# Kernel tuning notes

Hardware: AMD Instinct MI355X
Metric: run time of the kernel (lower is better)

Reference implementation:

```python
import jax, jax.numpy as jnp
import numpy as np

T, B, DX, DH, DZ, K = 128, 256, 64, 512, 128, 16


def _lin(x, W, b):
    return x @ W.T + b


def _forget_mult(F, Z, h0):
    # C[t] = F[t]*Z[t] + (1-F[t])*C[t-1], C[-1] = h0; shapes (T,B,H)
    def step(c, fz):
        f, z = fz
        c = f * z + (1.0 - f) * c
        return c, c
    _, C = jax.lax.scan(step, h0, (F, Z))
    return C


def _qrnn_layer(X, W, b, h0):
    # window=1, output_gate=True, zoneout=0 (eval)
    Y = _lin(X, W, b)                      # (T,B,3H)
    Z, F, O = jnp.split(Y, 3, axis=-1)
    C = _forget_mult(jax.nn.sigmoid(F), jnp.tanh(Z), h0)
    return jax.nn.sigmoid(O) * C           # H


def _planar_flow(z, u, w, b):
    # z: (B,T,Dz); u,w: (K,Dz); b: (K,). Returns z_K and summed log-det.
    def m(x):
        return jax.nn.softplus(x) - 1.0
    def step(carry, p):
        z, sldj = carry
        uk, wk, bk = p
        udw = jnp.dot(uk, wk)
        w_hat = wk / jnp.linalg.norm(wk)
        u_hat = (m(udw) - udw) * w_hat + uk
        t = jnp.tanh(z @ wk + bk)          # (B,T)
        z = z + u_hat * t[..., None]
        psi_u = (1.0 - t * t) * jnp.dot(wk, u_hat)
        sldj = sldj - jnp.log(jnp.abs(psi_u + 1.0) + 1e-8)
        return (z, sldj), None
    sldj0 = jnp.zeros(z.shape[:-1], z.dtype)
    (zK, sldj), _ = jax.lax.scan(step, (z, sldj0), (u, w, b))
    return zK, sldj


def _forward(x, y, eps, hs_W, hs_b, q_W, q_b, enc_phi_W, enc_phi_b,
             enc_mean_W, enc_mean_b, enc_std_W, enc_std_b,
             prior_phi_W, prior_phi_b, prior_mean_W, prior_mean_b,
             prior_std_W, prior_std_b, dec_phi_W1, dec_phi_b1,
             dec_phi_W2, dec_phi_b2, dec_mean_W, dec_mean_b,
             dec_std_W, dec_std_b, pnf_u, pnf_w, pnf_b):
    Bsz = x.shape[1]
    Dh = hs_W.shape[0] // 3
    h0 = jnp.zeros((Bsz, Dh), x.dtype)
    # hidden-state QRNN over x
    h = _qrnn_layer(x, hs_W, hs_b, h0)                 # (T,B,Dh)
    # inference QRNN over reversed [y, h]
    rev_in = jnp.concatenate([jnp.flip(y, 0), jnp.flip(h, 0)], axis=-1)
    a = _qrnn_layer(rev_in, q_W, q_b, h0)              # (T,B,Dh)
    rev_a = jnp.swapaxes(jnp.flip(a, 0), 0, 1)         # (B,T,Dh)
    # encoder
    e = jax.nn.relu(_lin(rev_a, enc_phi_W[0], enc_phi_b[0]))
    e = jax.nn.relu(_lin(e, enc_phi_W[1], enc_phi_b[1]))
    enc_mean = jax.nn.sigmoid(_lin(e, enc_mean_W, enc_mean_b))   # (B,T,Dz)
    enc_std = jax.nn.softplus(_lin(e, enc_std_W, enc_std_b))
    z0 = enc_mean + enc_std * eps
    z_k, sldj = _planar_flow(z0, pnf_u, pnf_w, pnf_b)
    # prior
    hp = jnp.swapaxes(h, 0, 1)                          # (B,T,Dh)
    p = jax.nn.relu(_lin(hp, prior_phi_W[0], prior_phi_b[0]))
    p = jax.nn.relu(_lin(p, prior_phi_W[1], prior_phi_b[1]))
    prior_mean = jax.nn.sigmoid(_lin(p, prior_mean_W, prior_mean_b))
    prior_std = jax.nn.softplus(_lin(p, prior_std_W, prior_std_b))
    # decoder
    d = jax.nn.relu(_lin(jnp.concatenate([z_k, hp], axis=-1), dec_phi_W1, dec_phi_b1))
    d = jax.nn.relu(_lin(d, dec_phi_W2, dec_phi_b2))
    dec_mean = jax.nn.sigmoid(_lin(d, dec_mean_W, dec_mean_b))   # (B,T,Dx)
    dec_std = jax.nn.softplus(_lin(d, dec_std_W, dec_std_b))
    return dec_mean, dec_std, enc_mean, enc_std, prior_mean, prior_std, z_k, sldj


def setup_inputs() -> dict:
    key = jax.random.key(0)
    ks = jax.random.split(key, 20)
    def w(i, shape, scale=0.05):
        return (jax.random.normal(ks[i], shape) * scale).astype(jnp.float32)
    return {
        "x": w(0, (T, B, DX), 1.0),
        "y": w(1, (T, B, DX), 1.0),
        "eps": w(2, (B, T, DZ), 1.0),
        "hs_W": w(3, (3 * DH, DX)), "hs_b": jnp.zeros((3 * DH,), jnp.float32),
        "q_W": w(4, (3 * DH, DX + DH)), "q_b": jnp.zeros((3 * DH,), jnp.float32),
        "enc_phi_W": w(5, (2, DH, DH)), "enc_phi_b": jnp.zeros((2, DH), jnp.float32),
        "enc_mean_W": w(6, (DZ, DH)), "enc_mean_b": jnp.zeros((DZ,), jnp.float32),
        "enc_std_W": w(7, (DZ, DH)), "enc_std_b": jnp.zeros((DZ,), jnp.float32),
        "prior_phi_W": w(8, (2, DH, DH)), "prior_phi_b": jnp.zeros((2, DH), jnp.float32),
        "prior_mean_W": w(9, (DZ, DH)), "prior_mean_b": jnp.zeros((DZ,), jnp.float32),
        "prior_std_W": w(10, (DZ, DH)), "prior_std_b": jnp.zeros((DZ,), jnp.float32),
        "dec_phi_W1": w(11, (DH, DH + DZ)), "dec_phi_b1": jnp.zeros((DH,), jnp.float32),
        "dec_phi_W2": w(12, (DH, DH)), "dec_phi_b2": jnp.zeros((DH,), jnp.float32),
        "dec_mean_W": w(13, (DX, DH)), "dec_mean_b": jnp.zeros((DX,), jnp.float32),
        "dec_std_W": w(14, (DX, DH)), "dec_std_b": jnp.zeros((DX,), jnp.float32),
        "pnf_u": w(15, (K, DZ), 0.01), "pnf_w": w(16, (K, DZ), 0.01), "pnf_b": w(17, (K,), 0.01),
    }


def reference(x, y, eps, hs_W, hs_b, q_W, q_b, enc_phi_W, enc_phi_b,
              enc_mean_W, enc_mean_b, enc_std_W, enc_std_b,
              prior_phi_W, prior_phi_b, prior_mean_W, prior_mean_b,
              prior_std_W, prior_std_b, dec_phi_W1, dec_phi_b1,
              dec_phi_W2, dec_phi_b2, dec_mean_W, dec_mean_b,
              dec_std_W, dec_std_b, pnf_u, pnf_w, pnf_b):
    return _forward(x, y, eps, hs_W, hs_b, q_W, q_b, enc_phi_W, enc_phi_b,
                    enc_mean_W, enc_mean_b, enc_std_W, enc_std_b,
                    prior_phi_W, prior_phi_b, prior_mean_W, prior_mean_b,
                    prior_std_W, prior_std_b, dec_phi_W1, dec_phi_b1,
                    dec_phi_W2, dec_phi_b2, dec_mean_W, dec_mean_b,
                    dec_std_W, dec_std_b, pnf_u, pnf_w, pnf_b)
```

## Files before the change

### kernel.cpp

```cpp
#include <hip/hip_runtime.h>
#include <cstddef>
#include <cstdint>

#define DEVI __device__ __forceinline__

namespace {

typedef _Float16 f16;
typedef _Float16 half4 __attribute__((ext_vector_type(4)));
typedef _Float16 half8 __attribute__((ext_vector_type(8)));
typedef _Float16 f16x2 __attribute__((ext_vector_type(2)));
typedef float floatx16 __attribute__((ext_vector_type(16)));

typedef const __attribute__((address_space(1))) void gvoid;
typedef __attribute__((address_space(3))) void lvoid;
#define GLL(gp, lp) __builtin_amdgcn_global_load_lds((gvoid*)(gp), (lvoid*)(lp), 16, 0, 0)

constexpr float kLog2e = 1.4426950408889634f;
constexpr float kLn2   = 0.6931471805599453f;
DEVI float fexp2_(float x) { return __builtin_amdgcn_exp2f(x); }
DEVI float frcp_(float x)  { return __builtin_amdgcn_rcpf(x); }
DEVI float flog2_(float x) { return __builtin_amdgcn_logf(x); }
DEVI float fsig_(float v)  { return frcp_(1.f + fexp2_(-kLog2e * v)); }
DEVI float ftanh_(float v) { return 1.f - 2.f * frcp_(1.f + fexp2_(2.f * kLog2e * v)); }
DEVI float fsoftplus_(float v) {
  return fmaxf(v, 0.f) + kLn2 * flog2_(1.f + fexp2_(-kLog2e * fabsf(v)));
}

struct CvtTab { const float* s[14]; f16* d[14]; int n4[14]; };

__global__ __launch_bounds__(256)
void cvt_k(CvtTab tab) {
  const int e = blockIdx.y;
  const int n4 = tab.n4[e];
  const float4* s = (const float4*)tab.s[e];
  f16* d = tab.d[e];
  for (int i = blockIdx.x * 256 + threadIdx.x; i < n4; i += gridDim.x * 256) {
    const float4 v = s[i];
    half4 o = {(f16)v.x, (f16)v.y, (f16)v.z, (f16)v.w};
    *(half4*)(d + (size_t)i * 4) = o;
  }
}

template <int AM, int OM>
__global__ __launch_bounds__(256)
void gemm16_k(const f16* __restrict__ A0, const f16* __restrict__ A1,
              const f16* __restrict__ W0, const f16* __restrict__ W1,
              const float* __restrict__ bias, const float* __restrict__ bias2,
              float* __restrict__ C, float* __restrict__ C2,
              f16* __restrict__ Ch, int N, int K, int lda) {
  __shared__ __align__(16) char lds[65536];
  const int tid = threadIdx.x;
  const int l = tid & 63, w = tid >> 6;
  const int m0 = blockIdx.y * 128, n0 = blockIdx.x * 128;
  const int Nh = N >> 1;

  const f16* pa[4]; const f16* pa2[4]; const f16* pb[4];
#pragma unroll
  for (int r = 0; r < 4; ++r) {
    const int s = w * 256 + r * 64 + l;
    const int row = s >> 3, c = s & 7;
    const int kc8 = (c ^ (row & 7)) * 8;
    const int m = m0 + row;
    if constexpr (AM == 0) {
      pa[r] = A0 + (size_t)m * lda + kc8;
      pa2[r] = nullptr;
    } else if constexpr (AM == 1) {
      const int t = m >> 8, b = m & 255;
      pa[r]  = A0 + (size_t)((127 - t) * 256 + b) * 64 + kc8;
      pa2[r] = A1 + (size_t)((b << 7) | (127 - t)) * 512 + kc8;
    } else {
      pa[r]  = A0 + (size_t)m * 128 + kc8;
      pa2[r] = A1 + (size_t)m * 512 + kc8;
    }
    const int n = n0 + row;
    if constexpr (OM == 2) {
      pb[r] = (n < Nh ? W0 + (size_t)n * K : W1 + (size_t)(n - Nh) * K) + kc8;
    } else {
      pb[r] = W0 + (size_t)n * K + kc8;
    }
  }

  const int wr0 = (w >> 1) * 64, wc0 = (w & 1) * 64;
  int offA[2][4], offB[2][4];
#pragma unroll
  for (int mi = 0; mi < 2; ++mi) {
    const int row = wr0 + mi * 32 + (l & 31);
#pragma unroll
    for (int s16 = 0; s16 < 4; ++s16) {
      const int c = (s16 * 2 + (l >> 5)) ^ (row & 7);
      offA[mi][s16] = row * 128 + c * 16;
    }
  }
#pragma unroll
  for (int nj = 0; nj < 2; ++nj) {
    const int row = wc0 + nj * 32 + (l & 31);
#pragma unroll
    for (int s16 = 0; s16 < 4; ++s16) {
      const int c = (s16 * 2 + (l >> 5)) ^ (row & 7);
      offB[nj][s16] = row * 128 + c * 16;
    }
  }

  float bv[2];
#pragma unroll
  for (int nj = 0; nj < 2; ++nj) {
    const int gcol = n0 + wc0 + nj * 32 + (l & 31);
    if constexpr (OM == 2) {
      bv[nj] = (gcol >= Nh) ? bias2[gcol - Nh] : bias[gcol];
    } else {
      bv[nj] = bias[gcol];
    }
  }
  asm volatile("" : "+v"(bv[0]), "+v"(bv[1]));
  asm volatile("s_waitcnt vmcnt(0)" ::: "memory");

  auto stage = [&](int st, int buf) {
    char* dA = lds + buf * 32768;
    char* dB = dA + 16384;
#pragma unroll
    for (int r = 0; r < 4; ++r) {
      const f16* ga;
      if constexpr (AM == 0)      ga = pa[r] + st * 64;
      else if constexpr (AM == 1) ga = (st == 0) ? pa[r] : (pa2[r] + (st - 1) * 64);
      else                        ga = (st < 2) ? (pa[r] + st * 64) : (pa2[r] + (st - 2) * 64);
      GLL(ga, dA + (w * 256 + r * 64) * 16);
      GLL(pb[r] + st * 64, dB + (w * 256 + r * 64) * 16);
    }
  };

  floatx16 acc[2][2] = {};
  const int nsteps = K >> 6;
  stage(0, 0);
  for (int st = 0; st < nsteps; ++st) {
    const int cur = st & 1;
    if (st + 1 < nsteps) {
      stage(st + 1, cur ^ 1);
      asm volatile("s_waitcnt vmcnt(8)" ::: "memory");
    } else {
      asm volatile("s_waitcnt vmcnt(0)" ::: "memory");
    }
    __builtin_amdgcn_s_barrier();
    __builtin_amdgcn_sched_barrier(0);
    const char* cA = lds + cur * 32768;
    const char* cB = cA + 16384;
#pragma unroll
    for (int s16 = 0; s16 < 4; ++s16) {
      const half8 a0 = *(const half8*)(cA + offA[0][s16]);
      const half8 a1 = *(const half8*)(cA + offA[1][s16]);
      const half8 b0 = *(const half8*)(cB + offB[0][s16]);
      const half8 b1 = *(const half8*)(cB + offB[1][s16]);
      acc[0][0] = __builtin_amdgcn_mfma_f32_32x32x16_f16(a0, b0, acc[0][0], 0, 0, 0);
      acc[0][1] = __builtin_amdgcn_mfma_f32_32x32x16_f16(a0, b1, acc[0][1], 0, 0, 0);
      acc[1][0] = __builtin_amdgcn_mfma_f32_32x32x16_f16(a1, b0, acc[1][0], 0, 0, 0);
      acc[1][1] = __builtin_amdgcn_mfma_f32_32x32x16_f16(a1, b1, acc[1][1], 0, 0, 0);
    }
    __builtin_amdgcn_sched_barrier(0);
    asm volatile("s_waitcnt lgkmcnt(0)" ::: "memory");
    __builtin_amdgcn_s_barrier();
  }

  const int col_l = l & 31;
#pragma unroll
  for (int nj = 0; nj < 2; ++nj) {
    const int gcol = n0 + wc0 + nj * 32 + col_l;
    if constexpr (OM == 2) {
      const bool second = gcol >= Nh;
      float* cp = second ? C2 : C;
      const int cl = second ? gcol - Nh : gcol;
#pragma unroll
      for (int mi = 0; mi < 2; ++mi) {
#pragma unroll
        for (int reg = 0; reg < 16; ++reg) {
          const int rl = (reg & 3) + 8 * (reg >> 2) + 4 * (l >> 5);
          const int grow = m0 + wr0 + mi * 32 + rl;
          const float v = acc[mi][nj][reg] + bv[nj];
          cp[(size_t)grow * Nh + cl] = second ? fsoftplus_(v) : fsig_(v);
        }
      }
    } else {
#pragma unroll
      for (int mi = 0; mi < 2; ++mi) {
#pragma unroll
        for (int reg = 0; reg < 16; ++reg) {
          const int rl = (reg & 3) + 8 * (reg >> 2) + 4 * (l >> 5);
          const int grow = m0 + wr0 + mi * 32 + rl;
          const float v = acc[mi][nj][reg] + bv[nj];
          float rr;
          if constexpr (OM == 0) rr = (gcol < 512) ? ftanh_(v) : fsig_(v);
          else                   rr = fmaxf(v, 0.f);
          Ch[(size_t)grow * N + gcol] = (f16)rr;
        }
      }
    }
  }
}

template <int MODE>
__global__ __launch_bounds__(256)
void scan_k(const f16* __restrict__ Y, f16* __restrict__ H1) {
  const int idx = blockIdx.x * 256 + threadIdx.x;
  const int b = idx >> 8;
  const int h0 = (idx & 255) * 2;
  float c0 = 0.f, c1 = 0.f;
  for (int t = 0; t < 128; ++t) {
    const f16* p = Y + (size_t)(t * 256 + b) * 1536 + h0;
    const f16x2 zv = *(const f16x2*)(p);
    const f16x2 fv = *(const f16x2*)(p + 512);
    const f16x2 ov = *(const f16x2*)(p + 1024);
    const float f0 = (float)fv[0], f1 = (float)fv[1];
    c0 = f0 * (float)zv[0] + (1.f - f0) * c0;
    c1 = f1 * (float)zv[1] + (1.f - f1) * c1;
    f16x2 hv = {(f16)((float)ov[0] * c0), (f16)((float)ov[1] * c1)};
    const int tt = (MODE == 0) ? t : (127 - t);
    *(f16x2*)(H1 + (size_t)((b << 7) | tt) * 512 + h0) = hv;
  }
}

__global__ __launch_bounds__(256)
void z0_k(const float* __restrict__ mean, const float* __restrict__ sd,
          const float* __restrict__ eps, float* __restrict__ z) {
  const int i = blockIdx.x * 256 + threadIdx.x;
  const float4 m = ((const float4*)mean)[i];
  const float4 s = ((const float4*)sd)[i];
  const float4 e = ((const float4*)eps)[i];
  ((float4*)z)[i] = make_float4(m.x + s.x * e.x, m.y + s.y * e.y,
                                m.z + s.z * e.z, m.w + s.w * e.w);
}

__global__ __launch_bounds__(64)
void flow_pre_k(const float* __restrict__ u, const float* __restrict__ w,
                float* __restrict__ uhat, float* __restrict__ wu) {
  const int k = blockIdx.x, l = threadIdx.x;
  const float w0 = w[k * 128 + l], w1 = w[k * 128 + 64 + l];
  const float u0 = u[k * 128 + l], u1 = u[k * 128 + 64 + l];
  float nrm = w0 * w0 + w1 * w1;
  float udw = u0 * w0 + u1 * w1;
#pragma unroll
  for (int o = 32; o; o >>= 1) { nrm += __shfl_xor(nrm, o); udw += __shfl_xor(udw, o); }
  const float inv = 1.f / sqrtf(nrm);
  const float coef = (fsoftplus_(udw) - 1.f) - udw;
  const float uh0 = coef * (w0 * inv) + u0;
  const float uh1 = coef * (w1 * inv) + u1;
  uhat[k * 128 + l] = uh0;
  uhat[k * 128 + 64 + l] = uh1;
  float dwu = w0 * uh0 + w1 * uh1;
#pragma unroll
  for (int o = 32; o; o >>= 1) dwu += __shfl_xor(dwu, o);
  if (l == 0) wu[k] = dwu;
}

__global__ __launch_bounds__(256)
void flow_k(float* __restrict__ z, const float* __restrict__ w,
            const float* __restrict__ b, const float* __restrict__ uhat,
            const float* __restrict__ wu, float* __restrict__ sldj,
            f16* __restrict__ zh) {
  const int row = blockIdx.x * 4 + (threadIdx.x >> 6);
  const int l = threadIdx.x & 63;
  float* zp = z + (size_t)row * 128;
  float z0 = zp[l], z1 = zp[64 + l];
  float sl = 0.f;
#pragma unroll
  for (int k = 0; k < 16; ++k) {
    const float w0 = w[k * 128 + l], w1 = w[k * 128 + 64 + l];
    float s = z0 * w0 + z1 * w1;
#pragma unroll
    for (int o = 32; o; o >>= 1) s += __shfl_xor(s, o);
    const float t = ftanh_(s + b[k]);
    z0 += uhat[k * 128 + l] * t;
    z1 += uhat[k * 128 + 64 + l] * t;
    const float psi = (1.f - t * t) * wu[k];
    sl -= kLn2 * flog2_(fabsf(psi + 1.f) + 1e-8f);
  }
  zp[l] = z0;
  zp[64 + l] = z1;
  zh[(size_t)row * 128 + l] = (f16)z0;
  zh[(size_t)row * 128 + 64 + l] = (f16)z1;
  if (l == 0) sldj[row] = sl;
}

}

extern "C" void kernel_launch(void* const* d_in, const int* in_sizes, int n_in,
                              void* d_out, int out_size, void* d_ws, size_t ws_size,
                              hipStream_t stream) {
  const float* x           = (const float*)d_in[0];
  const float* y           = (const float*)d_in[1];
  const float* eps         = (const float*)d_in[2];
  const float* hs_b        = (const float*)d_in[4];
  const float* q_b         = (const float*)d_in[6];
  const float* enc_phi_b   = (const float*)d_in[8];
  const float* enc_mean_b  = (const float*)d_in[10];
  const float* enc_std_b   = (const float*)d_in[12];
  const float* prior_phi_b = (const float*)d_in[14];
  const float* prior_mean_b= (const float*)d_in[16];
  const float* prior_std_b = (const float*)d_in[18];
  const float* dec_b1      = (const float*)d_in[20];
  const float* dec_b2      = (const float*)d_in[22];
  const float* dec_mean_b  = (const float*)d_in[24];
  const float* dec_std_b   = (const float*)d_in[26];
  const float* pnf_u       = (const float*)d_in[27];
  const float* pnf_w       = (const float*)d_in[28];
  const float* pnf_b       = (const float*)d_in[29];

  float* out = (float*)d_out;
  float* dec_mean  = out;
  float* dec_std   = out + 2097152;
  float* enc_mean  = out + 4194304;
  float* enc_std   = out + 8388608;
  float* prior_mean= out + 12582912;
  float* prior_std = out + 16777216;
  float* zk        = out + 20971520;
  float* sldj      = out + 25165824;

  char* ws = (char*)d_ws;
  f16* Ybuf  = (f16*)(ws + 0);
  f16* e1    = (f16*)(ws + 0);
  f16* e2    = (f16*)(ws + 33554432);
  f16* arev  = (f16*)(ws + 100663296);
  f16* h_bt  = (f16*)(ws + 134217728);
  f16* zk_h  = (f16*)(ws + 167772160);
  f16* xh    = (f16*)(ws + 176160768);
  f16* yh    = (f16*)(ws + 180355072);
  f16* wbuf  = (f16*)(ws + 184549376);
  float* uhat= (float*)(ws + 190447616);
  float* wu  = (float*)(ws + 190455808);

  f16* w_hs   = wbuf + 0;
  f16* w_q    = wbuf + 98304;
  f16* w_ephi = wbuf + 983040;
  f16* w_emean= wbuf + 1507328;
  f16* w_estd = wbuf + 1572864;
  f16* w_pphi = wbuf + 1638400;
  f16* w_pmean= wbuf + 2162688;
  f16* w_pstd = wbuf + 2228224;
  f16* w_d1   = wbuf + 2293760;
  f16* w_d2   = wbuf + 2621440;
  f16* w_dmean= wbuf + 2883584;
  f16* w_dstd = wbuf + 2916352;

  CvtTab tab;
  const float* srcs[14] = {x, y, (const float*)d_in[3], (const float*)d_in[5],
                           (const float*)d_in[7], (const float*)d_in[9],
                           (const float*)d_in[11], (const float*)d_in[13],
                           (const float*)d_in[15], (const float*)d_in[17],
                           (const float*)d_in[19], (const float*)d_in[21],
                           (const float*)d_in[23], (const float*)d_in[25]};
  f16* dsts[14] = {xh, yh, w_hs, w_q, w_ephi, w_emean, w_estd, w_pphi,
                   w_pmean, w_pstd, w_d1, w_d2, w_dmean, w_dstd};
  const int ns[14] = {2097152, 2097152, 98304, 884736, 524288, 65536, 65536,
                      524288, 65536, 65536, 327680, 262144, 32768, 32768};
  for (int i = 0; i < 14; ++i) { tab.s[i] = srcs[i]; tab.d[i] = dsts[i]; tab.n4[i] = ns[i] >> 2; }
  cvt_k<<<dim3(128, 14), 256, 0, stream>>>(tab);

  const dim3 blk(256);

  gemm16_k<0, 0><<<dim3(12, 256), blk, 0, stream>>>(xh, nullptr, w_hs, nullptr,
      hs_b, nullptr, nullptr, nullptr, Ybuf, 1536, 64, 64);
  scan_k<0><<<256, blk, 0, stream>>>(Ybuf, h_bt);

  gemm16_k<1, 0><<<dim3(12, 256), blk, 0, stream>>>(yh, h_bt, w_q, nullptr,
      q_b, nullptr, nullptr, nullptr, Ybuf, 1536, 576, 0);
  scan_k<1><<<256, blk, 0, stream>>>(Ybuf, arev);

  gemm16_k<0, 1><<<dim3(4, 256), blk, 0, stream>>>(arev, nullptr, w_ephi, nullptr,
      enc_phi_b, nullptr, nullptr, nullptr, e1, 512, 512, 512);
  gemm16_k<0, 1><<<dim3(4, 256), blk, 0, stream>>>(e1, nullptr, w_ephi + 262144, nullptr,
      enc_phi_b + 512, nullptr, nullptr, nullptr, e2, 512, 512, 512);
  gemm16_k<0, 2><<<dim3(2, 256), blk, 0, stream>>>(e2, nullptr, w_emean, w_estd,
      enc_mean_b, enc_std_b, enc_mean, enc_std, nullptr, 256, 512, 512);
  z0_k<<<4096, blk, 0, stream>>>(enc_mean, enc_std, eps, zk);
  flow_pre_k<<<16, 64, 0, stream>>>(pnf_u, pnf_w, uhat, wu);
  flow_k<<<8192, blk, 0, stream>>>(zk, pnf_w, pnf_b, uhat, wu, sldj, zk_h);

  gemm16_k<0, 1><<<dim3(4, 256), blk, 0, stream>>>(h_bt, nullptr, w_pphi, nullptr,
      prior_phi_b, nullptr, nullptr, nullptr, e1, 512, 512, 512);
  gemm16_k<0, 1><<<dim3(4, 256), blk, 0, stream>>>(e1, nullptr, w_pphi + 262144, nullptr,
      prior_phi_b + 512, nullptr, nullptr, nullptr, e2, 512, 512, 512);
  gemm16_k<0, 2><<<dim3(2, 256), blk, 0, stream>>>(e2, nullptr, w_pmean, w_pstd,
      prior_mean_b, prior_std_b, prior_mean, prior_std, nullptr, 256, 512, 512);

  gemm16_k<2, 1><<<dim3(4, 256), blk, 0, stream>>>(zk_h, h_bt, w_d1, nullptr,
      dec_b1, nullptr, nullptr, nullptr, e1, 512, 640, 0);
  gemm16_k<0, 1><<<dim3(4, 256), blk, 0, stream>>>(e1, nullptr, w_d2, nullptr,
      dec_b2, nullptr, nullptr, nullptr, e2, 512, 512, 512);
  gemm16_k<0, 2><<<dim3(1, 256), blk, 0, stream>>>(e2, nullptr, w_dmean, w_dstd,
      dec_mean_b, dec_std_b, dec_mean, dec_std, nullptr, 128, 512, 512);
}
```

Baseline: 657.3 us.

## Enlarge GEMM tiles to 256x256 with 512 threads and XCD-aware block swizzle

The shared GEMM kernel moves from 128x128 tiles on 4 waves to 256x256 tiles on 8 waves. Each wave now computes a 128x64 subtile, which raises MFMA work per LDS fragment load, and LDS grows to 128KB for double buffering. Blocks use a 1D grid remapped so consecutive tiles land on the same XCD, which should improve L2 reuse. The cost is fewer workgroups: 128 to 768 per GEMM on 256 CUs, so tail and occupancy may suffer. It also adds clamping for the narrow mean/std GEMM (N=128) whose tile is wider than N.

```diff
diff --git a/kernel.cpp b/kernel.cpp
--- a/kernel.cpp
+++ b/kernel.cpp
@@ -43,22 +43,26 @@
 }
 
 template <int AM, int OM>
-__global__ __launch_bounds__(256)
+__global__ __launch_bounds__(512, 2)
 void gemm16_k(const f16* __restrict__ A0, const f16* __restrict__ A1,
               const f16* __restrict__ W0, const f16* __restrict__ W1,
               const float* __restrict__ bias, const float* __restrict__ bias2,
               float* __restrict__ C, float* __restrict__ C2,
-              f16* __restrict__ Ch, int N, int K, int lda) {
-  __shared__ __align__(16) char lds[65536];
+              f16* __restrict__ Ch, int N, int K, int lda, int ntx) {
+  __shared__ __align__(16) char lds[131072];
   const int tid = threadIdx.x;
   const int l = tid & 63, w = tid >> 6;
-  const int m0 = blockIdx.y * 128, n0 = blockIdx.x * 128;
+  const int nwg = gridDim.x;
+  int bid = blockIdx.x;
+  bid = (bid & 7) * (nwg >> 3) + (bid >> 3);
+  const int m0 = (bid / ntx) * 256;
+  const int n0 = (bid % ntx) * 256;
   const int Nh = N >> 1;
 
   const f16* pa[4]; const f16* pa2[4]; const f16* pb[4];
 #pragma unroll
   for (int r = 0; r < 4; ++r) {
-    const int s = w * 256 + r * 64 + l;
+    const int s = r * 512 + tid;
     const int row = s >> 3, c = s & 7;
     const int kc8 = (c ^ (row & 7)) * 8;
     const int m = m0 + row;
@@ -73,7 +77,8 @@
       pa[r]  = A0 + (size_t)m * 128 + kc8;
       pa2[r] = A1 + (size_t)m * 512 + kc8;
     }
-    const int n = n0 + row;
+    int n = n0 + row;
+    if constexpr (OM == 2) n = n < N ? n : N - 1;
     if constexpr (OM == 2) {
       pb[r] = (n < Nh ? W0 + (size_t)n * K : W1 + (size_t)(n - Nh) * K) + kc8;
     } else {
@@ -81,11 +86,11 @@
     }
   }
 
-  const int wr0 = (w >> 1) * 64, wc0 = (w & 1) * 64;
-  int offA[2][4], offB[2][4];
-#pragma unroll
-  for (int mi = 0; mi < 2; ++mi) {
-    const int row = wr0 + mi * 32 + (l & 31);
+  const int wr = w >> 2, wc = w & 3;
+  int offA[4][4], offB[2][4];
+#pragma unroll
+  for (int mi = 0; mi < 4; ++mi) {
+    const int row = wr * 128 + mi * 32 + (l & 31);
 #pragma unroll
     for (int s16 = 0; s16 < 4; ++s16) {
       const int c = (s16 * 2 + (l >> 5)) ^ (row & 7);
@@ -94,7 +99,7 @@
   }
 #pragma unroll
   for (int nj = 0; nj < 2; ++nj) {
-    const int row = wc0 + nj * 32 + (l & 31);
+    const int row = wc * 64 + nj * 32 + (l & 31);
 #pragma unroll
     for (int s16 = 0; s16 < 4; ++s16) {
       const int c = (s16 * 2 + (l >> 5)) ^ (row & 7);
@@ -105,9 +110,10 @@
   float bv[2];
 #pragma unroll
   for (int nj = 0; nj < 2; ++nj) {
-    const int gcol = n0 + wc0 + nj * 32 + (l & 31);
+    int gcol = n0 + wc * 64 + nj * 32 + (l & 31);
     if constexpr (OM == 2) {
-      bv[nj] = (gcol >= Nh) ? bias2[gcol - Nh] : bias[gcol];
+      const int gi = gcol < N ? gcol : N - 1;
+      bv[nj] = (gi >= Nh) ? bias2[gi - Nh] : bias[gi];
     } else {
       bv[nj] = bias[gcol];
     }
@@ -116,20 +122,20 @@
   asm volatile("s_waitcnt vmcnt(0)" ::: "memory");
 
   auto stage = [&](int st, int buf) {
-    char* dA = lds + buf * 32768;
-    char* dB = dA + 16384;
+    char* dA = lds + buf * 65536;
+    char* dB = dA + 32768;
 #pragma unroll
     for (int r = 0; r < 4; ++r) {
       const f16* ga;
       if constexpr (AM == 0)      ga = pa[r] + st * 64;
       else if constexpr (AM == 1) ga = (st == 0) ? pa[r] : (pa2[r] + (st - 1) * 64);
       else                        ga = (st < 2) ? (pa[r] + st * 64) : (pa2[r] + (st - 2) * 64);
-      GLL(ga, dA + (w * 256 + r * 64) * 16);
-      GLL(pb[r] + st * 64, dB + (w * 256 + r * 64) * 16);
+      GLL(ga, dA + (r * 512 + w * 64) * 16);
+      GLL(pb[r] + st * 64, dB + (r * 512 + w * 64) * 16);
     }
   };
 
-  floatx16 acc[2][2] = {};
+  floatx16 acc[4][2] = {};
   const int nsteps = K >> 6;
   stage(0, 0);
   for (int st = 0; st < nsteps; ++st) {
@@ -142,18 +148,24 @@
     }
     __builtin_amdgcn_s_barrier();
     __builtin_amdgcn_sched_barrier(0);
-    const char* cA = lds + cur * 32768;
-    const char* cB = cA + 16384;
+    const char* cA = lds + cur * 65536;
+    const char* cB = cA + 32768;
 #pragma unroll
     for (int s16 = 0; s16 < 4; ++s16) {
-      const half8 a0 = *(const half8*)(cA + offA[0][s16]);
-      const half8 a1 = *(const half8*)(cA + offA[1][s16]);
-      const half8 b0 = *(const half8*)(cB + offB[0][s16]);
-      const half8 b1 = *(const half8*)(cB + offB[1][s16]);
+      half8 a0 = *(const half8*)(cA + offA[0][s16]);
+      half8 a1 = *(const half8*)(cA + offA[1][s16]);
+      half8 a2 = *(const half8*)(cA + offA[2][s16]);
+      half8 a3 = *(const half8*)(cA + offA[3][s16]);
+      half8 b0 = *(const half8*)(cB + offB[0][s16]);
+      half8 b1 = *(const half8*)(cB + offB[1][s16]);
       acc[0][0] = __builtin_amdgcn_mfma_f32_32x32x16_f16(a0, b0, acc[0][0], 0, 0, 0);
       acc[0][1] = __builtin_amdgcn_mfma_f32_32x32x16_f16(a0, b1, acc[0][1], 0, 0, 0);
       acc[1][0] = __builtin_amdgcn_mfma_f32_32x32x16_f16(a1, b0, acc[1][0], 0, 0, 0);
       acc[1][1] = __builtin_amdgcn_mfma_f32_32x32x16_f16(a1, b1, acc[1][1], 0, 0, 0);
+      acc[2][0] = __builtin_amdgcn_mfma_f32_32x32x16_f16(a2, b0, acc[2][0], 0, 0, 0);
+      acc[2][1] = __builtin_amdgcn_mfma_f32_32x32x16_f16(a2, b1, acc[2][1], 0, 0, 0);
+      acc[3][0] = __builtin_amdgcn_mfma_f32_32x32x16_f16(a3, b0, acc[3][0], 0, 0, 0);
+      acc[3][1] = __builtin_amdgcn_mfma_f32_32x32x16_f16(a3, b1, acc[3][1], 0, 0, 0);
     }
     __builtin_amdgcn_sched_barrier(0);
     asm volatile("s_waitcnt lgkmcnt(0)" ::: "memory");
@@ -161,30 +173,33 @@
   }
 
   const int col_l = l & 31;
+  const int hi4 = (l >> 5) * 4;
 #pragma unroll
   for (int nj = 0; nj < 2; ++nj) {
-    const int gcol = n0 + wc0 + nj * 32 + col_l;
+    const int gcol = n0 + wc * 64 + nj * 32 + col_l;
     if constexpr (OM == 2) {
-      const bool second = gcol >= Nh;
-      float* cp = second ? C2 : C;
-      const int cl = second ? gcol - Nh : gcol;
-#pragma unroll
-      for (int mi = 0; mi < 2; ++mi) {
-#pragma unroll
-        for (int reg = 0; reg < 16; ++reg) {
-          const int rl = (reg & 3) + 8 * (reg >> 2) + 4 * (l >> 5);
-          const int grow = m0 + wr0 + mi * 32 + rl;
-          const float v = acc[mi][nj][reg] + bv[nj];
-          cp[(size_t)grow * Nh + cl] = second ? fsoftplus_(v) : fsig_(v);
+      if (gcol < N) {
+        const bool second = gcol >= Nh;
+        float* cp = second ? C2 : C;
+        const int cl = second ? gcol - Nh : gcol;
+#pragma unroll
+        for (int mi = 0; mi < 4; ++mi) {
+#pragma unroll
+          for (int reg = 0; reg < 16; ++reg) {
+            const int rl = (reg & 3) + 8 * (reg >> 2) + hi4;
+            const int grow = m0 + wr * 128 + mi * 32 + rl;
+            const float v = acc[mi][nj][reg] + bv[nj];
+            cp[(size_t)grow * Nh + cl] = second ? fsoftplus_(v) : fsig_(v);
+          }
         }
       }
     } else {
 #pragma unroll
-      for (int mi = 0; mi < 2; ++mi) {
+      for (int mi = 0; mi < 4; ++mi) {
 #pragma unroll
         for (int reg = 0; reg < 16; ++reg) {
-          const int rl = (reg & 3) + 8 * (reg >> 2) + 4 * (l >> 5);
-          const int grow = m0 + wr0 + mi * 32 + rl;
+          const int rl = (reg & 3) + 8 * (reg >> 2) + hi4;
+          const int grow = m0 + wr * 128 + mi * 32 + rl;
           const float v = acc[mi][nj][reg] + bv[nj];
           float rr;
           if constexpr (OM == 0) rr = (gcol < 512) ? ftanh_(v) : fsig_(v);
@@ -353,37 +368,37 @@
   for (int i = 0; i < 14; ++i) { tab.s[i] = srcs[i]; tab.d[i] = dsts[i]; tab.n4[i] = ns[i] >> 2; }
   cvt_k<<<dim3(128, 14), 256, 0, stream>>>(tab);
 
-  const dim3 blk(256);
-
-  gemm16_k<0, 0><<<dim3(12, 256), blk, 0, stream>>>(xh, nullptr, w_hs, nullptr,
-      hs_b, nullptr, nullptr, nullptr, Ybuf, 1536, 64, 64);
-  scan_k<0><<<256, blk, 0, stream>>>(Ybuf, h_bt);
-
-  gemm16_k<1, 0><<<dim3(12, 256), blk, 0, stream>>>(yh, h_bt, w_q, nullptr,
-      q_b, nullptr, nullptr, nullptr, Ybuf, 1536, 576, 0);
-  scan_k<1><<<256, blk, 0, stream>>>(Ybuf, arev);
-
-  gemm16_k<0, 1><<<dim3(4, 256), blk, 0, stream>>>(arev, nullptr, w_ephi, nullptr,
-      enc_phi_b, nullptr, nullptr, nullptr, e1, 512, 512, 512);
-  gemm16_k<0, 1><<<dim3(4, 256), blk, 0, stream>>>(e1, nullptr, w_ephi + 262144, nullptr,
-      enc_phi_b + 512, nullptr, nullptr, nullptr, e2, 512, 512, 512);
-  gemm16_k<0, 2><<<dim3(2, 256), blk, 0, stream>>>(e2, nullptr, w_emean, w_estd,
-      enc_mean_b, enc_std_b, enc_mean, enc_std, nullptr, 256, 512, 512);
-  z0_k<<<4096, blk, 0, stream>>>(enc_mean, enc_std, eps, zk);
+  const dim3 blk(512);
+
+  gemm16_k<0, 0><<<768, blk, 0, stream>>>(xh, nullptr, w_hs, nullptr,
+      hs_b, nullptr, nullptr, nullptr, Ybuf, 1536, 64, 64, 6);
+  scan_k<0><<<256, 256, 0, stream>>>(Ybuf, h_bt);
+
+  gemm16_k<1, 0><<<768, blk, 0, stream>>>(yh, h_bt, w_q, nullptr,
+      q_b, nullptr, nullptr, nullptr, Ybuf, 1536, 576, 0, 6);
+  scan_k<1><<<256, 256, 0, stream>>>(Ybuf, arev);
+
+  gemm16_k<0, 1><<<256, blk, 0, stream>>>(arev, nullptr, w_ephi, nullptr,
+      enc_phi_b, nullptr, nullptr, nullptr, e1, 512, 512, 512, 2);
+  gemm16_k<0, 1><<<256, blk, 0, stream>>>(e1, nullptr, w_ephi + 262144, nullptr,
+      enc_phi_b + 512, nullptr, nullptr, nullptr, e2, 512, 512, 512, 2);
+  gemm16_k<0, 2><<<128, blk, 0, stream>>>(e2, nullptr, w_emean, w_estd,
+      enc_mean_b, enc_std_b, enc_mean, enc_std, nullptr, 256, 512, 512, 1);
+  z0_k<<<4096, 256, 0, stream>>>(enc_mean, enc_std, eps, zk);
   flow_pre_k<<<16, 64, 0, stream>>>(pnf_u, pnf_w, uhat, wu);
-  flow_k<<<8192, blk, 0, stream>>>(zk, pnf_w, pnf_b, uhat, wu, sldj, zk_h);
-
-  gemm16_k<0, 1><<<dim3(4, 256), blk, 0, stream>>>(h_bt, nullptr, w_pphi, nullptr,
-      prior_phi_b, nullptr, nullptr, nullptr, e1, 512, 512, 512);
-  gemm16_k<0, 1><<<dim3(4, 256), blk, 0, stream>>>(e1, nullptr, w_pphi + 262144, nullptr,
-      prior_phi_b + 512, nullptr, nullptr, nullptr, e2, 512, 512, 512);
-  gemm16_k<0, 2><<<dim3(2, 256), blk, 0, stream>>>(e2, nullptr, w_pmean, w_pstd,
-      prior_mean_b, prior_std_b, prior_mean, prior_std, nullptr, 256, 512, 512);
-
-  gemm16_k<2, 1><<<dim3(4, 256), blk, 0, stream>>>(zk_h, h_bt, w_d1, nullptr,
-      dec_b1, nullptr, nullptr, nullptr, e1, 512, 640, 0);
-  gemm16_k<0, 1><<<dim3(4, 256), blk, 0, stream>>>(e1, nullptr, w_d2, nullptr,
-      dec_b2, nullptr, nullptr, nullptr, e2, 512, 512, 512);
-  gemm16_k<0, 2><<<dim3(1, 256), blk, 0, stream>>>(e2, nullptr, w_dmean, w_dstd,
-      dec_mean_b, dec_std_b, dec_mean, dec_std, nullptr, 128, 512, 512);
-}
+  flow_k<<<8192, 256, 0, stream>>>(zk, pnf_w, pnf_b, uhat, wu, sldj, zk_h);
+
+  gemm16_k<0, 1><<<256, blk, 0, stream>>>(h_bt, nullptr, w_pphi, nullptr,
+      prior_phi_b, nullptr, nullptr, nullptr, e1, 512, 512, 512, 2);
+  gemm16_k<0, 1><<<256, blk, 0, stream>>>(e1, nullptr, w_pphi + 262144, nullptr,
+      prior_phi_b + 512, nullptr, nullptr, nullptr, e2, 512, 512, 512, 2);
+  gemm16_k<0, 2><<<128, blk, 0, stream>>>(e2, nullptr, w_pmean, w_pstd,
+      prior_mean_b, prior_std_b, prior_mean, prior_std, nullptr, 256, 512, 512, 1);
+
+  gemm16_k<2, 1><<<256, blk, 0, stream>>>(zk_h, h_bt, w_d1, nullptr,
+      dec_b1, nullptr, nullptr, nullptr, e1, 512, 640, 0, 2);
+  gemm16_k<0, 1><<<256, blk, 0, stream>>>(e1, nullptr, w_d2, nullptr,
+      dec_b2, nullptr, nullptr, nullptr, e2, 512, 512, 512, 2);
+  gemm16_k<0, 2><<<128, blk, 0, stream>>>(e2, nullptr, w_dmean, w_dstd,
+      dec_mean_b, dec_std_b, dec_mean, dec_std, nullptr, 128, 512, 512, 1);
+}
```

Measured after the change: 649.3 us. No clear change (-1.2%).
